# Kernel tuning notes

Hardware: AMD Instinct MI355X
Metric: run time of the kernel (lower is better)

The kernel has to match this reference:

```python
import jax, jax.numpy as jnp
import numpy as np

L, N, D, V, K = 512, 65536, 128, 21, 9  # seq len, n mutations, hidden, vocab, conv kernel


def setup_inputs() -> dict:
    key = jax.random.key(0)
    ks = jax.random.split(key, 24)
    # wildtype sequence and single-point mutants (guaranteed one mismatch each)
    wt = jax.random.randint(ks[0], (L,), 0, V, dtype=jnp.int32)
    pos = jax.random.randint(ks[1], (N,), 0, L)
    delta = jax.random.randint(ks[2], (N,), 1, V)
    muts = jnp.tile(wt[None, :], (N, 1))
    muts = muts.at[jnp.arange(N), pos].set(((wt[pos] + delta) % V).astype(jnp.int32))

    def lin(k, o, i):
        return jax.random.normal(k, (o, i), dtype=jnp.float32) / np.float32(np.sqrt(i))

    return {
        "all_input": jax.random.normal(ks[3], (L, D), dtype=jnp.float32),
        "seqs": wt[None, :],                      # [1, L]
        "sortcery_seqs": muts[None],              # [1, N, L]
        "sortcery_nrgs": jax.random.normal(ks[4], (1, N), dtype=jnp.float32),
        # LightAttention conv weights (torch Conv1d layout [out, in, k])
        "Wf": jax.random.normal(ks[5], (D, D, K), dtype=jnp.float32) / np.float32(np.sqrt(D * K)),
        "bf": jnp.zeros((D,), jnp.float32),
        "Wa": jax.random.normal(ks[6], (D, D, K), dtype=jnp.float32) / np.float32(np.sqrt(D * K)),
        "ba": jnp.zeros((D,), jnp.float32),
        # MLP: ReLU->Linear chain, sizes 128->128->64->32->21 (torch layout [out, in])
        "W1": lin(ks[7], 128, 128), "b1": jnp.zeros((128,), jnp.float32),
        "W2": lin(ks[8], 64, 128),  "b2": jnp.zeros((64,), jnp.float32),
        "W3": lin(ks[9], 32, 64),   "b3": jnp.zeros((32,), jnp.float32),
        "W4": lin(ks[10], 21, 32),  "b4": jnp.zeros((21,), jnp.float32),
        # ddg_out: Linear(1,1)
        "Wd": jax.random.normal(ks[11], (1, 1), dtype=jnp.float32),
        "bd": jnp.zeros((1,), jnp.float32),
    }


def _forward(all_input, sortcery_nrgs, Wf, bf, Wa, ba, W1, b1, W2, b2, W3, b3, W4, b4, Wd, bd,
             seqs, sortcery_seqs):
    wt = seqs[0]                                   # [L]
    muts = sortcery_seqs[0]                        # [N, L]
    mism = muts != wt[None, :]                     # [N, L]
    pos = jnp.argmax(mism, axis=1)                 # first mismatch position per mutation
    valid = jnp.any(mism, axis=1)                  # loop 'continue' when no mismatch

    x = all_input[pos]                             # [N, D] -- the length-1 conv input
    c = K // 2
    # Conv1d(k=9, pad=4) on a length-1 sequence: only the center tap sees nonzero input.
    feat = x @ Wf[:, :, c].T + bf                  # [N, D]
    att = x @ Wa[:, :, c].T + ba                   # [N, D]
    # softmax over the length-1 sequence axis is identically 1
    p = jax.nn.softmax(att[..., None], axis=-1)[..., 0]
    h = feat * p

    for W, b in ((W1, b1), (W2, b2), (W3, b3), (W4, b4)):
        h = jnp.maximum(h, 0.0) @ W.T + b
    logits = h                                     # [N, V]

    ddg_out = logits * Wd[0, 0] + bd[0]            # Linear(1,1) applied elementwise: [N, V]
    wc = wt[pos]                                   # wildtype char at mismatch
    mc = jnp.take_along_axis(muts, pos[:, None], axis=1)[:, 0]  # mutant char
    ddg = (jnp.take_along_axis(ddg_out, wc[:, None], axis=1)
           - jnp.take_along_axis(ddg_out, mc[:, None], axis=1))[:, 0]  # [N]

    preds = jnp.where(valid, ddg, 0.0)
    reals = jnp.where(valid, sortcery_nrgs[0], 0.0)
    return preds, reals


def reference(all_input, seqs, sortcery_seqs, sortcery_nrgs, Wf, bf, Wa, ba,
              W1, b1, W2, b2, W3, b3, W4, b4, Wd, bd):
    return _forward(all_input, sortcery_nrgs, Wf, bf, Wa, ba,
                    W1, b1, W2, b2, W3, b3, W4, b4, Wd, bd, seqs, sortcery_seqs)
```

## Files before the change

### kernel.cpp

```cpp
#include <hip/hip_runtime.h>

#define LSEQ 512
#define NMUT 65536
#define DDIM 128
#define VOCAB 21
#define KCONV 9
#define DDS 48
#define TPB 8
#define NB_TAB (LSEQ / TPB)
#define RPW 8
#define NB_SCAN (NMUT / (4 * RPW))
#define W4OFF 2080

#define RESOLVE2(A, W, BP)                                                     \
    {                                                                          \
        const int dx = (A).x - (W).x, dy = (A).y - (W).y;                      \
        const unsigned long long msk = __ballot((dx | dy) != 0);               \
        if (msk) {                                                             \
            const int j = dx ? 0 : 1;                                          \
            const int d = dx ? dx : dy;                                        \
            const int cand = ((d + 32) << 10) | ((BP) + 2 * lane + j);         \
            res[k] = __shfl(cand, __ffsll(msk) - 1);                           \
        }                                                                      \
    }

__global__ __launch_bounds__(256) void fused_kernel(
    const float* __restrict__ all_input,
    const int*   __restrict__ wt,
    const int*   __restrict__ muts,
    const float* __restrict__ Wf, const float* __restrict__ bf,
    const float* __restrict__ W1, const float* __restrict__ b1,
    const float* __restrict__ W2, const float* __restrict__ b2,
    const float* __restrict__ W3, const float* __restrict__ b3,
    const float* __restrict__ W4, const float* __restrict__ b4,
    const float* __restrict__ Wd, const float* __restrict__ bd,
    float* __restrict__ tabDD,
    int*   __restrict__ meta)
{
    __shared__ float Wl[4224];
    __shared__ float xa[DDIM][TPB];
    __shared__ float xb[DDIM][TPB];
    const int tid = threadIdx.x;

    if (blockIdx.x < NB_TAB) {
        const int p0 = blockIdx.x * TPB;
        const int ph = tid >> 7;
        const int o  = tid & 127;

        #pragma unroll
        for (int k = 0; k < 4; ++k) {
            const int f = tid + k * 256;
            xa[f & 127][f >> 7] = all_input[p0 * DDIM + f];
        }

        float4 acc;
        { const float b = bf[o]; acc = make_float4(b, b, b, b); }
        #pragma unroll
        for (int q = 0; q < 4; ++q) {
            __syncthreads();
            #pragma unroll
            for (int it = 0; it < 16; ++it) {
                const int e = tid + it * 256;
                const int row = e >> 5, col = e & 31;
                Wl[row * 33 + col] =
                    Wf[(row * DDIM + q * 32 + col) * KCONV + KCONV / 2];
            }
            __syncthreads();
            #pragma unroll
            for (int j = 0; j < 32; ++j) {
                const float w = Wl[o * 33 + j];
                const float4 x = *(const float4*)&xa[q * 32 + j][ph * 4];
                acc.x = fmaf(x.x, w, acc.x);
                acc.y = fmaf(x.y, w, acc.y);
                acc.z = fmaf(x.z, w, acc.z);
                acc.w = fmaf(x.w, w, acc.w);
            }
        }
        xb[o][ph * 4 + 0] = fmaxf(acc.x, 0.f);
        xb[o][ph * 4 + 1] = fmaxf(acc.y, 0.f);
        xb[o][ph * 4 + 2] = fmaxf(acc.z, 0.f);
        xb[o][ph * 4 + 3] = fmaxf(acc.w, 0.f);

        { const float b = b1[o]; acc = make_float4(b, b, b, b); }
        #pragma unroll
        for (int q = 0; q < 4; ++q) {
            __syncthreads();
            #pragma unroll
            for (int it = 0; it < 16; ++it) {
                const int e = tid + it * 256;
                const int row = e >> 5, col = e & 31;
                Wl[row * 33 + col] = W1[row * DDIM + q * 32 + col];
            }
            __syncthreads();
            #pragma unroll
            for (int j = 0; j < 32; ++j) {
                const float w = Wl[o * 33 + j];
                const float4 x = *(const float4*)&xb[q * 32 + j][ph * 4];
                acc.x = fmaf(x.x, w, acc.x);
                acc.y = fmaf(x.y, w, acc.y);
                acc.z = fmaf(x.z, w, acc.z);
                acc.w = fmaf(x.w, w, acc.w);
            }
        }
        xa[o][ph * 4 + 0] = fmaxf(acc.x, 0.f);
        xa[o][ph * 4 + 1] = fmaxf(acc.y, 0.f);
        xa[o][ph * 4 + 2] = fmaxf(acc.z, 0.f);
        xa[o][ph * 4 + 3] = fmaxf(acc.w, 0.f);

        float4 a3;
        { const float b = (o < 64) ? b2[o] : 0.f; a3 = make_float4(b, b, b, b); }
        #pragma unroll
        for (int h = 0; h < 2; ++h) {
            __syncthreads();
            #pragma unroll
            for (int it = 0; it < 16; ++it) {
                const int e = tid + it * 256;
                const int row = e >> 6, col = e & 63;
                Wl[row * 65 + col] = W2[row * DDIM + h * 64 + col];
            }
            __syncthreads();
            if (o < 64) {
                #pragma unroll
                for (int j = 0; j < 64; ++j) {
                    const float w = Wl[o * 65 + j];
                    const float4 x = *(const float4*)&xa[h * 64 + j][ph * 4];
                    a3.x = fmaf(x.x, w, a3.x);
                    a3.y = fmaf(x.y, w, a3.y);
                    a3.z = fmaf(x.z, w, a3.z);
                    a3.w = fmaf(x.w, w, a3.w);
                }
            }
        }
        if (o < 64) {
            xb[o][ph * 4 + 0] = fmaxf(a3.x, 0.f);
            xb[o][ph * 4 + 1] = fmaxf(a3.y, 0.f);
            xb[o][ph * 4 + 2] = fmaxf(a3.z, 0.f);
            xb[o][ph * 4 + 3] = fmaxf(a3.w, 0.f);
        }
        __syncthreads();

        for (int e = tid; e < 2048; e += 256)
            Wl[(e >> 6) * 65 + (e & 63)] = W3[e];
        for (int e = tid; e < 672; e += 256)
            Wl[W4OFF + (e >> 5) * 33 + (e & 31)] = W4[e];
        __syncthreads();

        if (o < 32) {
            float4 a4;
            { const float b = b3[o]; a4 = make_float4(b, b, b, b); }
            #pragma unroll
            for (int j = 0; j < 64; ++j) {
                const float w = Wl[o * 65 + j];
                const float4 x = *(const float4*)&xb[j][ph * 4];
                a4.x = fmaf(x.x, w, a4.x);
                a4.y = fmaf(x.y, w, a4.y);
                a4.z = fmaf(x.z, w, a4.z);
                a4.w = fmaf(x.w, w, a4.w);
            }
            xa[o][ph * 4 + 0] = fmaxf(a4.x, 0.f);
            xa[o][ph * 4 + 1] = fmaxf(a4.y, 0.f);
            xa[o][ph * 4 + 2] = fmaxf(a4.z, 0.f);
            xa[o][ph * 4 + 3] = fmaxf(a4.w, 0.f);
        }
        __syncthreads();

        if (o < VOCAB) {
            const float wd = Wd[0], bdv = bd[0];
            float4 a5;
            { const float b = b4[o]; a5 = make_float4(b, b, b, b); }
            #pragma unroll
            for (int j = 0; j < 32; ++j) {
                const float w = Wl[W4OFF + o * 33 + j];
                const float4 x = *(const float4*)&xa[j][ph * 4];
                a5.x = fmaf(x.x, w, a5.x);
                a5.y = fmaf(x.y, w, a5.y);
                a5.z = fmaf(x.z, w, a5.z);
                a5.w = fmaf(x.w, w, a5.w);
            }
            xb[o][ph * 4 + 0] = a5.x * wd + bdv;
            xb[o][ph * 4 + 1] = a5.y * wd + bdv;
            xb[o][ph * 4 + 2] = a5.z * wd + bdv;
            xb[o][ph * 4 + 3] = a5.w * wd + bdv;
        }
        __syncthreads();

        for (int e = tid; e < TPB * 41; e += 256) {
            const int pl = e / 41;
            const int j  = e - pl * 41;
            const int wc = wt[p0 + pl];
            const int mc = wc + j - 20;
            float v = 0.f;
            if (mc >= 0 && mc < VOCAB)
                v = xb[wc][pl] - xb[mc][pl];
            tabDD[(p0 + pl) * DDS + j] = v;
        }
        return;
    }

    const int lane  = tid & 63;
    const int sbid  = blockIdx.x - NB_TAB;
    const int rbase = (sbid * 4 + (tid >> 6)) * RPW;

    const int2* __restrict__ wt2 = (const int2*)wt;
    const int2 w0 = wt2[lane];
    const int2 w1 = wt2[64 + lane];
    const int2 w2 = wt2[128 + lane];
    const int2 w3 = wt2[192 + lane];
    const int2* __restrict__ base = (const int2*)muts + (size_t)rbase * (LSEQ / 2);

    int res[RPW];
    int2 a[RPW];

    #pragma unroll
    for (int k = 0; k < RPW; ++k)
        a[k] = base[(size_t)k * (LSEQ / 2) + lane];
    #pragma unroll
    for (int k = 0; k < RPW; ++k) {
        res[k] = -1;
        RESOLVE2(a[k], w0, 0);
    }

    #pragma unroll
    for (int k = 0; k < RPW; ++k)
        if (res[k] < 0) a[k] = base[(size_t)k * (LSEQ / 2) + 64 + lane];
    #pragma unroll
    for (int k = 0; k < RPW; ++k)
        if (res[k] < 0) RESOLVE2(a[k], w1, 128);

    #pragma unroll
    for (int k = 0; k < RPW; ++k)
        if (res[k] < 0) a[k] = base[(size_t)k * (LSEQ / 2) + 128 + lane];
    #pragma unroll
    for (int k = 0; k < RPW; ++k)
        if (res[k] < 0) RESOLVE2(a[k], w2, 256);

    #pragma unroll
    for (int k = 0; k < RPW; ++k)
        if (res[k] < 0) a[k] = base[(size_t)k * (LSEQ / 2) + 192 + lane];
    #pragma unroll
    for (int k = 0; k < RPW; ++k)
        if (res[k] < 0) RESOLVE2(a[k], w3, 384);

    int myres = -1;
    #pragma unroll
    for (int k = 0; k < RPW; ++k)
        if (lane == k) myres = res[k];
    if (lane < RPW)
        meta[rbase + lane] = myres;
}

__global__ __launch_bounds__(256) void lookup_kernel(
    const int*   __restrict__ meta,
    const float* __restrict__ tabDD,
    const float* __restrict__ nrgs,
    float* __restrict__ preds,
    float* __restrict__ reals)
{
    const int r = blockIdx.x * 256 + threadIdx.x;
    const int m = meta[r];
    float pred = 0.f, real = 0.f;
    if (m >= 0) {
        const int pos = m & 1023;
        const int d0  = (m >> 10) - 32;
        pred = tabDD[pos * DDS + d0 + 20];
        real = nrgs[r];
    }
    preds[r] = pred;
    reals[r] = real;
}

extern "C" void kernel_launch(void* const* d_in, const int* in_sizes, int n_in,
                              void* d_out, int out_size, void* d_ws, size_t ws_size,
                              hipStream_t stream) {
    const float* all_input = (const float*)d_in[0];
    const int*   seqs      = (const int*)  d_in[1];
    const int*   muts      = (const int*)  d_in[2];
    const float* nrgs      = (const float*)d_in[3];
    const float* Wf        = (const float*)d_in[4];
    const float* bf        = (const float*)d_in[5];
    const float* W1 = (const float*)d_in[8];
    const float* b1 = (const float*)d_in[9];
    const float* W2 = (const float*)d_in[10];
    const float* b2 = (const float*)d_in[11];
    const float* W3 = (const float*)d_in[12];
    const float* b3 = (const float*)d_in[13];
    const float* W4 = (const float*)d_in[14];
    const float* b4 = (const float*)d_in[15];
    const float* Wd = (const float*)d_in[16];
    const float* bd = (const float*)d_in[17];

    char* ws = (char*)d_ws;
    float* tabDD = (float*)ws;  ws += LSEQ * DDS * 4;
    int*   meta  = (int*)ws;
    float* preds = (float*)d_out;
    float* reals = (float*)d_out + NMUT;

    fused_kernel<<<NB_TAB + NB_SCAN, 256, 0, stream>>>(
        all_input, seqs, muts,
        Wf, bf, W1, b1, W2, b2, W3, b3, W4, b4, Wd, bd,
        tabDD, meta);

    lookup_kernel<<<NMUT / 256, 256, 0, stream>>>(meta, tabDD, nrgs, preds, reals);
}
```

Measured before the change: 31.24 us.

## Fuse lookup into main kernel via global atomic completion barrier

Removes the second lookup kernel launch. The 64 table blocks now spin on a global atomic counter until every block (table and scan) has finished, then perform the meta/tabDD lookup and write preds/reals for their slice. This saves a kernel launch and its dependency gap, but adds a hipMemsetAsync per call and a spin-wait. The spin relies on all 2112 blocks being co-resident or the table blocks being scheduled first, so it risks deadlock or idle waiting CUs.

Measured after the change: 91.89 us. +194.1%, slower.

```diff
diff --git a/kernel.cpp b/kernel.cpp
--- a/kernel.cpp
+++ b/kernel.cpp
@@ -10,6 +10,7 @@
 #define NB_TAB (LSEQ / TPB)
 #define RPW 8
 #define NB_SCAN (NMUT / (4 * RPW))
+#define NB_ALL (NB_TAB + NB_SCAN)
 #define W4OFF 2080
 
 #define RESOLVE2(A, W, BP)                                                     \
@@ -28,6 +29,7 @@
     const float* __restrict__ all_input,
     const int*   __restrict__ wt,
     const int*   __restrict__ muts,
+    const float* __restrict__ nrgs,
     const float* __restrict__ Wf, const float* __restrict__ bf,
     const float* __restrict__ W1, const float* __restrict__ b1,
     const float* __restrict__ W2, const float* __restrict__ b2,
@@ -35,7 +37,10 @@
     const float* __restrict__ W4, const float* __restrict__ b4,
     const float* __restrict__ Wd, const float* __restrict__ bd,
     float* __restrict__ tabDD,
-    int*   __restrict__ meta)
+    int*   __restrict__ meta,
+    unsigned int* __restrict__ done_ctr,
+    float* __restrict__ preds,
+    float* __restrict__ reals)
 {
     __shared__ float Wl[4224];
     __shared__ float xa[DDIM][TPB];
@@ -194,6 +199,32 @@
                 v = xb[wc][pl] - xb[mc][pl];
             tabDD[(p0 + pl) * DDS + j] = v;
         }
+
+        __syncthreads();
+        if (tid == 0) {
+            __threadfence();
+            atomicAdd(done_ctr, 1u);
+            while (atomicAdd(done_ctr, 0u) < (unsigned)NB_ALL)
+                __builtin_amdgcn_s_sleep(8);
+            __threadfence();
+        }
+        __syncthreads();
+
+        const int rbase = blockIdx.x * (NMUT / NB_TAB);
+        #pragma unroll
+        for (int it = 0; it < (NMUT / NB_TAB) / 256; ++it) {
+            const int r = rbase + it * 256 + tid;
+            const int m = meta[r];
+            float pred = 0.f, real = 0.f;
+            if (m >= 0) {
+                const int pos = m & 1023;
+                const int d0  = (m >> 10) - 32;
+                pred = tabDD[pos * DDS + d0 + 20];
+                real = nrgs[r];
+            }
+            preds[r] = pred;
+            reals[r] = real;
+        }
         return;
     }
 
@@ -247,26 +278,12 @@
         if (lane == k) myres = res[k];
     if (lane < RPW)
         meta[rbase + lane] = myres;
-}
-
-__global__ __launch_bounds__(256) void lookup_kernel(
-    const int*   __restrict__ meta,
-    const float* __restrict__ tabDD,
-    const float* __restrict__ nrgs,
-    float* __restrict__ preds,
-    float* __restrict__ reals)
-{
-    const int r = blockIdx.x * 256 + threadIdx.x;
-    const int m = meta[r];
-    float pred = 0.f, real = 0.f;
-    if (m >= 0) {
-        const int pos = m & 1023;
-        const int d0  = (m >> 10) - 32;
-        pred = tabDD[pos * DDS + d0 + 20];
-        real = nrgs[r];
+
+    __syncthreads();
+    if (tid == 0) {
+        __threadfence();
+        atomicAdd(done_ctr, 1u);
     }
-    preds[r] = pred;
-    reals[r] = real;
 }
 
 extern "C" void kernel_launch(void* const* d_in, const int* in_sizes, int n_in,
@@ -290,15 +307,16 @@
     const float* bd = (const float*)d_in[17];
 
     char* ws = (char*)d_ws;
-    float* tabDD = (float*)ws;  ws += LSEQ * DDS * 4;
-    int*   meta  = (int*)ws;
+    float* tabDD = (float*)ws;            ws += LSEQ * DDS * 4;
+    int*   meta  = (int*)ws;              ws += NMUT * 4;
+    unsigned int* done_ctr = (unsigned int*)ws;
     float* preds = (float*)d_out;
     float* reals = (float*)d_out + NMUT;
 
-    fused_kernel<<<NB_TAB + NB_SCAN, 256, 0, stream>>>(
-        all_input, seqs, muts,
+    hipMemsetAsync(done_ctr, 0, 4, stream);
+
+    fused_kernel<<<NB_ALL, 256, 0, stream>>>(
+        all_input, seqs, muts, nrgs,
         Wf, bf, W1, b1, W2, b2, W3, b3, W4, b4, Wd, bd,
-        tabDD, meta);
-
-    lookup_kernel<<<NMUT / 256, 256, 0, stream>>>(meta, tabDD, nrgs, preds, reals);
+        tabDD, meta, done_ctr, preds, reals);
 }
```
